# Performance work log

Measured on AMD Instinct MI355X. Metric: run time of the kernel, lower is better.

Reference implementation:

```python
import jax, jax.numpy as jnp
import numpy as np

N, E = 50000, 500000          # nodes per type, edges per message type
F_IN, H, L = 128, 128, 8      # input feat, hidden_size, num_labels
EPS, SLOPE = 1e-5, 0.01       # BatchNorm eps, LeakyReLU slope


def setup_inputs() -> dict:
    key = jax.random.key(0)
    ks = jax.random.split(key, 16)
    s = 0.05
    d = {}
    d["x_n0"] = jax.random.normal(ks[0], (N, F_IN), jnp.float32)
    d["x_n1"] = jax.random.normal(ks[1], (N, F_IN), jnp.float32)
    # stacked per-message-type SAGE params (3 message types), two layers
    d["Wn1"] = jax.random.normal(ks[2], (3, F_IN, H), jnp.float32) * s
    d["Ws1"] = jax.random.normal(ks[3], (3, F_IN, H), jnp.float32) * s
    d["Wu1"] = jax.random.normal(ks[4], (3, 2 * H, H), jnp.float32) * s
    d["Wn2"] = jax.random.normal(ks[5], (3, H, H), jnp.float32) * s
    d["Ws2"] = jax.random.normal(ks[6], (3, H, H), jnp.float32) * s
    d["Wu2"] = jax.random.normal(ks[7], (3, 2 * H, H), jnp.float32) * s
    for nm in ("bn1", "bs1", "bu1", "bn2", "bs2", "bu2"):
        d[nm] = jnp.zeros((3, H), jnp.float32)
    # per-node-type BatchNorm affine params (2 node types), two layers
    d["gamma1"] = jnp.ones((2, H), jnp.float32)
    d["beta1"] = jnp.zeros((2, H), jnp.float32)
    d["gamma2"] = jnp.ones((2, H), jnp.float32)
    d["beta2"] = jnp.zeros((2, H), jnp.float32)
    # per-node-type post-MP linear
    d["Wp"] = jax.random.normal(ks[8], (2, H, L), jnp.float32) * s
    d["bp"] = jnp.zeros((2, L), jnp.float32)
    # edge_index per message type: [2, E] with row0=src, row1=dst
    d["ei0"] = jax.random.randint(ks[9], (2, E), 0, N, jnp.int32)   # n0 -> n1
    d["ei1"] = jax.random.randint(ks[10], (2, E), 0, N, jnp.int32)  # n1 -> n0
    d["ei2"] = jax.random.randint(ks[11], (2, E), 0, N, jnp.int32)  # n0 -> n0
    return d


def _segment_mean(x, idx, n):
    s = jax.ops.segment_sum(x, idx, num_segments=n)
    c = jax.ops.segment_sum(jnp.ones((idx.shape[0], 1), x.dtype), idx, num_segments=n)
    return s / jnp.maximum(c, 1.0)


def _sage(x_src, x_dst, ei, Wn, bn, Ws, bs, Wu, bu):
    # gather source feats per edge, scatter-mean to dst, then linear branches
    agg = _segment_mean(x_src[ei[0]], ei[1], x_dst.shape[0])  # [N_dst, F]
    h = jnp.concatenate([agg @ Wn + bn, x_dst @ Ws + bs], axis=-1)
    return h @ Wu + bu


def _bn(x, g, b):
    m = x.mean(0)
    v = ((x - m) ** 2).mean(0)  # biased variance, as torch BN training mode
    return (x - m) * jax.lax.rsqrt(v + EPS) * g + b


def _lrelu(x):
    return jnp.where(x >= 0, x, SLOPE * x)


def _layer(x0, x1, ei0, ei1, ei2, Wn, bn, Ws, bs, Wu, bu, gamma, beta):
    m0 = _sage(x0, x1, ei0, Wn[0], bn[0], Ws[0], bs[0], Wu[0], bu[0])  # dst n1
    m1 = _sage(x1, x0, ei1, Wn[1], bn[1], Ws[1], bs[1], Wu[1], bu[1])  # dst n0
    m2 = _sage(x0, x0, ei2, Wn[2], bn[2], Ws[2], bs[2], Wu[2], bu[2])  # dst n0
    h0 = 0.5 * (m1 + m2)   # mean over the 2 message types targeting n0
    h1 = m0                # single message type for n1
    h0 = _lrelu(_bn(h0, gamma[0], beta[0]))
    h1 = _lrelu(_bn(h1, gamma[1], beta[1]))
    return h0, h1


def reference(x_n0, x_n1, Wn1, bn1, Ws1, bs1, Wu1, bu1,
              Wn2, bn2, Ws2, bs2, Wu2, bu2,
              gamma1, beta1, gamma2, beta2, Wp, bp, ei0, ei1, ei2):
    h0, h1 = _layer(x_n0, x_n1, ei0, ei1, ei2, Wn1, bn1, Ws1, bs1, Wu1, bu1, gamma1, beta1)
    h0, h1 = _layer(h0, h1, ei0, ei1, ei2, Wn2, bn2, Ws2, bs2, Wu2, bu2, gamma2, beta2)
    out0 = h0 @ Wp[0] + bp[0]
    out1 = h1 @ Wp[1] + bp[1]
    return jnp.stack([out0, out1])  # [2, N, L]
```

## Files before the change

### kernel.cpp

```cpp
#include <hip/hip_runtime.h>

#define LBL 8
#define NBMAX 128
#define BSH 9
#define BCAP 8192

typedef __attribute__((ext_vector_type(8))) short short8;
typedef __attribute__((ext_vector_type(4))) float f32x4;

__device__ __forceinline__ uint f2bf(float x) {
    uint u = __float_as_uint(x);
    return (u + 0x7fffu + ((u >> 16) & 1u)) >> 16;
}
__device__ __forceinline__ float bflo(uint v) { return __uint_as_float(v << 16); }
__device__ __forceinline__ float bfhi(uint v) { return __uint_as_float(v & 0xffff0000u); }

__device__ __forceinline__ void gload16(const ushort* g, ushort* l) {
    __builtin_amdgcn_global_load_lds((const __attribute__((address_space(1))) uint*)g,
                                     (__attribute__((address_space(3))) uint*)l, 16, 0, 0);
}

__global__ void f2b2(const float4* __restrict__ x0, const float4* __restrict__ x1,
                     uint2* __restrict__ o0, uint2* __restrict__ o1, int n4) {
    int y = blockIdx.y;
    const float4* in = y ? x1 : x0;
    uint2* out = y ? o1 : o0;
    int i = blockIdx.x * blockDim.x + threadIdx.x;
    int stride = gridDim.x * blockDim.x;
    for (; i < n4; i += stride) {
        float4 v = in[i];
        uint2 o;
        o.x = f2bf(v.x) | (f2bf(v.y) << 16);
        o.y = f2bf(v.z) | (f2bf(v.w) << 16);
        out[i] = o;
    }
}


__global__ void bhist3(const int* __restrict__ e0, const int* __restrict__ e1,
                       const int* __restrict__ e2, int E, int NB, int* __restrict__ bcnt) {
    int m = blockIdx.y;
    const int* dst = (m == 0 ? e0 : (m == 1 ? e1 : e2)) + E;
    __shared__ int h[NBMAX];
    int tid = threadIdx.x;
    if (tid < NB) h[tid] = 0;
    __syncthreads();
    int i = blockIdx.x * blockDim.x + tid, st = gridDim.x * blockDim.x;
    for (; i < E; i += st) atomicAdd(&h[dst[i] >> BSH], 1);
    __syncthreads();
    if (tid < NB && h[tid]) atomicAdd(&bcnt[m * NB + tid], h[tid]);
}

__global__ void bscan(const int* __restrict__ bcnt, int* __restrict__ bso,
                      int* __restrict__ gcur, int NB) {
    int m = threadIdx.x;
    if (m >= 3) return;
    int acc = 0;
    for (int b = 0; b < NB; ++b) {
        bso[m * (NB + 1) + b] = acc;
        gcur[m * NB + b] = acc;
        acc += bcnt[m * NB + b];
    }
    bso[m * (NB + 1) + NB] = acc;
}

#define BIN_CH 16
__global__ __launch_bounds__(256) void bin3(const int* __restrict__ e0, const int* __restrict__ e1,
                                            const int* __restrict__ e2, int E, int NB,
                                            int* __restrict__ gcur, uint* __restrict__ pairs) {
    int m = blockIdx.y;
    const int* eb = (m == 0 ? e0 : (m == 1 ? e1 : e2));
    const int* src = eb;
    const int* dst = eb + E;
    uint* pp = pairs + (size_t)m * E;
    int* gc = gcur + m * NB;
    __shared__ int h[NBMAX], base[NBMAX], pos[NBMAX];
    int tid = threadIdx.x;
    if (tid < NB) { h[tid] = 0; pos[tid] = 0; }
    __syncthreads();
    int i0 = blockIdx.x * (256 * BIN_CH);
    uint pk[BIN_CH];
    int bk[BIN_CH];
    #pragma unroll
    for (int u = 0; u < BIN_CH; ++u) {
        int i = i0 + u * 256 + tid;
        bk[u] = -1;
        if (i < E) {
            int s = src[i], d = dst[i];
            bk[u] = d >> BSH;
            pk[u] = (uint)s | ((uint)(d & ((1 << BSH) - 1)) << 16);
            atomicAdd(&h[bk[u]], 1);
        }
    }
    __syncthreads();
    if (tid < NB && h[tid]) base[tid] = atomicAdd(&gc[tid], h[tid]);
    __syncthreads();
    #pragma unroll
    for (int u = 0; u < BIN_CH; ++u) {
        if (bk[u] >= 0) {
            int p = base[bk[u]] + atomicAdd(&pos[bk[u]], 1);
            pp[p] = pk[u];
        }
    }
}

__global__ __launch_bounds__(256) void csr3(const uint* __restrict__ pairs, const int* __restrict__ bso,
                                            int E, int N, int NB,
                                            int* __restrict__ offs, ushort* __restrict__ srcs) {
    int m = blockIdx.y, b = blockIdx.x;
    const uint* pp = pairs + (size_t)m * E;
    int gstart = bso[m * (NB + 1) + b];
    int gend = bso[m * (NB + 1) + b + 1];
    int cnt = gend - gstart;
    if (cnt > BCAP) cnt = BCAP;
    int d0 = b << BSH;
    int dcnt = N - d0;
    if (dcnt > (1 << BSH)) dcnt = 1 << BSH;

    __shared__ int hist[1 << BSH], po[1 << BSH], off0[1 << BSH];
    __shared__ int lsort[BCAP];
    __shared__ int wsum[4];
    int tid = threadIdx.x;
    hist[tid] = 0;
    hist[tid + 256] = 0;
    __syncthreads();
    for (int i = tid; i < cnt; i += 256) atomicAdd(&hist[pp[gstart + i] >> 16], 1);
    __syncthreads();
    int a = hist[2 * tid], b2 = hist[2 * tid + 1];
    int s = a + b2;
    int lane = tid & 63, w = tid >> 6;
    #pragma unroll
    for (int o = 1; o < 64; o <<= 1) {
        int v = __shfl_up(s, o, 64);
        if (lane >= o) s += v;
    }
    if (lane == 63) wsum[w] = s;
    __syncthreads();
    int wp = 0;
    #pragma unroll
    for (int q = 0; q < 4; ++q)
        if (q < w) wp += wsum[q];
    int excl = wp + s - a - b2;
    off0[2 * tid] = excl; off0[2 * tid + 1] = excl + a;
    po[2 * tid] = excl;   po[2 * tid + 1] = excl + a;
    __syncthreads();
    for (int j = tid; j < dcnt; j += 256) offs[(size_t)m * (N + 1) + d0 + j] = gstart + off0[j];
    if (b == NB - 1 && tid == 0) offs[(size_t)m * (N + 1) + N] = bso[m * (NB + 1) + NB];
    for (int i = tid; i < cnt; i += 256) {
        uint e = pp[gstart + i];
        int p = atomicAdd(&po[e >> 16], 1);
        if (p < BCAP) lsort[p] = (int)(e & 0xffffu);
    }
    __syncthreads();
    for (int i = tid; i < cnt; i += 256) srcs[(size_t)m * E + gstart + i] = (ushort)lsort[i];
}

__global__ void agg3(const ushort* __restrict__ s0, const ushort* __restrict__ s1,
                     const ushort* __restrict__ s2,
                     uint* __restrict__ o0, uint* __restrict__ o1, uint* __restrict__ o2,
                     const int* __restrict__ offs, const ushort* __restrict__ srcs,
                     int n, int E) {
    int m = blockIdx.y;
    const uint4* x = (const uint4*)(m == 0 ? s0 : (m == 1 ? s1 : s2));
    uint4* o = (uint4*)(m == 0 ? o0 : (m == 1 ? o1 : o2));
    const int* off = offs + (size_t)m * (n + 1);
    const ushort* sl = srcs + (size_t)m * E;

    int tid = threadIdx.x;
    int l16 = tid & 15;
    int row = blockIdx.x * 16 + (tid >> 4);
    if (row >= n) return;
    int s = off[row], e = off[row + 1];
    float a0 = 0, a1 = 0, a2 = 0, a3 = 0, a4 = 0, a5 = 0, a6 = 0, a7 = 0;
    int i = s;
    for (; i + 3 < e; i += 4) {
        int j0 = sl[i], j1 = sl[i + 1], j2 = sl[i + 2], j3 = sl[i + 3];
        uint4 v0 = x[(size_t)j0 * 16 + l16];
        uint4 v1 = x[(size_t)j1 * 16 + l16];
        uint4 v2 = x[(size_t)j2 * 16 + l16];
        uint4 v3 = x[(size_t)j3 * 16 + l16];
        a0 += (bflo(v0.x) + bflo(v1.x)) + (bflo(v2.x) + bflo(v3.x));
        a1 += (bfhi(v0.x) + bfhi(v1.x)) + (bfhi(v2.x) + bfhi(v3.x));
        a2 += (bflo(v0.y) + bflo(v1.y)) + (bflo(v2.y) + bflo(v3.y));
        a3 += (bfhi(v0.y) + bfhi(v1.y)) + (bfhi(v2.y) + bfhi(v3.y));
        a4 += (bflo(v0.z) + bflo(v1.z)) + (bflo(v2.z) + bflo(v3.z));
        a5 += (bfhi(v0.z) + bfhi(v1.z)) + (bfhi(v2.z) + bfhi(v3.z));
        a6 += (bflo(v0.w) + bflo(v1.w)) + (bflo(v2.w) + bflo(v3.w));
        a7 += (bfhi(v0.w) + bfhi(v1.w)) + (bfhi(v2.w) + bfhi(v3.w));
    }
    for (; i < e; ++i) {
        uint4 v = x[(size_t)sl[i] * 16 + l16];
        a0 += bflo(v.x); a1 += bfhi(v.x);
        a2 += bflo(v.y); a3 += bfhi(v.y);
        a4 += bflo(v.z); a5 += bfhi(v.z);
        a6 += bflo(v.w); a7 += bfhi(v.w);
    }
    int d = e - s;
    float inv = 1.f / (float)(d > 0 ? d : 1);
    uint4 r;
    r.x = f2bf(a0 * inv) | (f2bf(a1 * inv) << 16);
    r.y = f2bf(a2 * inv) | (f2bf(a3 * inv) << 16);
    r.z = f2bf(a4 * inv) | (f2bf(a5 * inv) << 16);
    r.w = f2bf(a6 * inv) | (f2bf(a7 * inv) << 16);
    o[(size_t)row * 16 + l16] = r;
}

__global__ void fuseW(const float* __restrict__ Wn1, const float* __restrict__ Ws1,
                      const float* __restrict__ Wu1,
                      const float* __restrict__ Wn2, const float* __restrict__ Ws2,
                      const float* __restrict__ Wu2, ushort* __restrict__ FT) {
    int j5 = blockIdx.y;
    int l = j5 / 5, t = j5 - l * 5;
    const float* Wn = l ? Wn2 : Wn1;
    const float* Ws = l ? Ws2 : Ws1;
    const float* Wu = l ? Wu2 : Wu1;
    const float *A0, *B0, *A1 = nullptr, *B1 = nullptr;
    float al;
    switch (t) {
        case 0: A0 = Wn;          B0 = Wu;          al = 1.0f; break;
        case 1: A0 = Wn + 16384;  B0 = Wu + 32768;  al = 0.5f; break;
        case 2: A0 = Wn + 32768;  B0 = Wu + 65536;  al = 0.5f; break;
        case 3: A0 = Ws;          B0 = Wu + 16384;  al = 1.0f; break;
        default:
            A0 = Ws + 16384; B0 = Wu + 49152;
            A1 = Ws + 32768; B1 = Wu + 81920;
            al = 0.5f; break;
    }
    int i = blockIdx.x, j = threadIdx.x;
    float s0 = 0, s1 = 0, s2 = 0, s3 = 0;
    #pragma unroll 4
    for (int k = 0; k < 128; k += 4) {
        s0 += A0[i * 128 + k]     * B0[k * 128 + j];
        s1 += A0[i * 128 + k + 1] * B0[(k + 1) * 128 + j];
        s2 += A0[i * 128 + k + 2] * B0[(k + 2) * 128 + j];
        s3 += A0[i * 128 + k + 3] * B0[(k + 3) * 128 + j];
    }
    if (A1) {
        #pragma unroll 4
        for (int k = 0; k < 128; k += 4) {
            s0 += A1[i * 128 + k]     * B1[k * 128 + j];
            s1 += A1[i * 128 + k + 1] * B1[(k + 1) * 128 + j];
            s2 += A1[i * 128 + k + 2] * B1[(k + 2) * 128 + j];
            s3 += A1[i * 128 + k + 3] * B1[(k + 3) * 128 + j];
        }
    }
    float r = al * ((s0 + s1) + (s2 + s3));
    FT[(size_t)j5 * 16384 + j * 128 + i] = (ushort)f2bf(r);
}

__global__ void fuseB(const float* __restrict__ bn1, const float* __restrict__ bs1,
                      const float* __restrict__ bu1, const float* __restrict__ Wu1,
                      const float* __restrict__ bn2, const float* __restrict__ bs2,
                      const float* __restrict__ bu2, const float* __restrict__ Wu2,
                      float* __restrict__ FC) {
    int jb = blockIdx.x;
    int l = jb >> 1, which = jb & 1;
    const float* bn = l ? bn2 : bn1;
    const float* bs = l ? bs2 : bs1;
    const float* bu = l ? bu2 : bu1;
    const float* Wu = l ? Wu2 : Wu1;
    int j = threadIdx.x;
    float s = 0.f;
    if (which == 0) {
        s = bu[j];
        for (int k = 0; k < 128; ++k)
            s += bn[k] * Wu[k * 128 + j] + bs[k] * Wu[(128 + k) * 128 + j];
    } else {
        #pragma unroll
        for (int tt = 1; tt <= 2; ++tt) {
            const float* Wt = Wu + tt * 32768;
            float p = bu[tt * 128 + j];
            for (int k = 0; k < 128; ++k)
                p += bn[tt * 128 + k] * Wt[k * 128 + j] + bs[tt * 128 + k] * Wt[(128 + k) * 128 + j];
            s += 0.5f * p;
        }
    }
    FC[jb * 128 + j] = s;
}

__global__ __launch_bounds__(256) void gemm2_mfma(
    const ushort* __restrict__ Aq0, const ushort* __restrict__ Wq0,
    const ushort* __restrict__ Aq1, const ushort* __restrict__ Wq1,
    const ushort* __restrict__ Ap0, const ushort* __restrict__ Wp0,
    const ushort* __restrict__ Ap1, const ushort* __restrict__ Wp1,
    const ushort* __restrict__ Ap2, const ushort* __restrict__ Wp2,
    const float* __restrict__ biasq, const float* __restrict__ biasp,
    ushort* __restrict__ Cq, ushort* __restrict__ Cp, int M,
    float* __restrict__ STW) {
    __shared__ ushort As[2][64 * 128];
    int y = blockIdx.y;
    const float* bias = y ? biasp : biasq;
    ushort* C = y ? Cp : Cq;
    float* colsum = STW + (size_t)(blockIdx.x & 31) * 512 + (y ? 0 : 256);
    float* colsq = colsum + 128;

    int tid = threadIdx.x;
    int wid = tid >> 6;
    int lane = tid & 63;
    int l15 = lane & 15, lg = lane >> 4;
    int row0 = blockIdx.x * 64;
    int nIn = y ? 3 : 2;

    const ushort* Ax[3];
    const ushort* Wx[3];
    Ax[0] = y ? Ap0 : Aq0;  Wx[0] = y ? Wp0 : Wq0;
    Ax[1] = y ? Ap1 : Aq1;  Wx[1] = y ? Wp1 : Wq1;
    Ax[2] = Ap2;            Wx[2] = Wp2;

    auto stage = [&](const ushort* A, ushort* buf) {
        #pragma unroll
        for (int p = 0; p < 4; ++p) {
            int row = wid * 16 + p * 4 + (lane >> 4);
            int gr = row0 + row;
            if (gr > M - 1) gr = M - 1;
            const ushort* src = A + (size_t)gr * 128 + (((lane & 15) ^ (row & 7)) * 8);
            gload16(src, buf + (wid * 4 + p) * 512);
        }
    };

    f32x4 acc[4][2];
    #pragma unroll
    for (int rb = 0; rb < 4; ++rb)
        #pragma unroll
        for (int cb = 0; cb < 2; ++cb) acc[rb][cb] = (f32x4){0.f, 0.f, 0.f, 0.f};

    stage(Ax[0], As[0]);
    __syncthreads();
    int cur = 0;

    #pragma unroll
    for (int inp = 0; inp < 3; ++inp) {
        if (inp == 2 && nIn == 2) break;
        const ushort* W = Wx[inp];
        short8 bw[4][2];
        #pragma unroll
        for (int k0 = 0; k0 < 4; ++k0)
            #pragma unroll
            for (int cb = 0; cb < 2; ++cb)
                bw[k0][cb] = *(const short8*)(W + (size_t)(wid * 32 + cb * 16 + l15) * 128 + k0 * 32 + lg * 8);
        if (inp + 1 < nIn) stage(Ax[inp + 1], As[cur ^ 1]);
        #pragma unroll
        for (int k0 = 0; k0 < 4; ++k0) {
            short8 a[4];
            #pragma unroll
            for (int rb = 0; rb < 4; ++rb)
                a[rb] = *(const short8*)&As[cur][(rb * 16 + l15) * 128 + (((k0 * 4 + lg) ^ (l15 & 7)) * 8)];
            #pragma unroll
            for (int rb = 0; rb < 4; ++rb)
                #pragma unroll
                for (int cb = 0; cb < 2; ++cb)
                    acc[rb][cb] = __builtin_amdgcn_mfma_f32_16x16x32_bf16(a[rb], bw[k0][cb], acc[rb][cb], 0, 0, 0);
        }
        __syncthreads();
        cur ^= 1;
    }

    float ps[2] = {0.f, 0.f}, pq[2] = {0.f, 0.f};
    int colbase = wid * 32;
    ushort* T = As[0];
    #pragma unroll
    for (int cb = 0; cb < 2; ++cb) {
        int col = colbase + cb * 16 + l15;
        float b = bias[col];
        #pragma unroll
        for (int rb = 0; rb < 4; ++rb) {
            int lrow = rb * 16 + lg * 4;
            #pragma unroll
            for (int i = 0; i < 4; ++i) {
                float v = acc[rb][cb][i] + b;
                T[(lrow + i) * 128 + col] = (ushort)f2bf(v);
                if (row0 + lrow + i < M) {
                    ps[cb] += v;
                    pq[cb] += v * v;
                }
            }
        }
    }
    #pragma unroll
    for (int cb = 0; cb < 2; ++cb) {
        ps[cb] += __shfl_xor(ps[cb], 16, 64);
        ps[cb] += __shfl_xor(ps[cb], 32, 64);
        pq[cb] += __shfl_xor(pq[cb], 16, 64);
        pq[cb] += __shfl_xor(pq[cb], 32, 64);
    }
    if (lane < 16) {
        atomicAdd(&colsum[colbase + lane], ps[0]);
        atomicAdd(&colsq[colbase + lane], pq[0]);
        atomicAdd(&colsum[colbase + 16 + lane], ps[1]);
        atomicAdd(&colsq[colbase + 16 + lane], pq[1]);
    }
    __syncthreads();
    {
        int row = tid >> 2;
        int c0 = (tid & 3) * 32;
        int gr = row0 + row;
        if (gr < M) {
            uint4* dst = (uint4*)(C + (size_t)gr * 128 + c0);
            const uint4* src4 = (const uint4*)&T[row * 128 + c0];
            dst[0] = src4[0];
            dst[1] = src4[1];
            dst[2] = src4[2];
            dst[3] = src4[3];
        }
    }
}

__global__ void bn_fin2(float* __restrict__ STW, float* __restrict__ ST,
                        const float* __restrict__ g0, const float* __restrict__ b0,
                        const float* __restrict__ g1, const float* __restrict__ b1, int N) {
    int tid = threadIdx.x;
    int which = tid >> 7, c = tid & 127;
    float s = 0.f, q = 0.f;
    #pragma unroll 8
    for (int cp = 0; cp < 32; ++cp) {
        s += STW[(size_t)cp * 512 + which * 256 + c];
        q += STW[(size_t)cp * 512 + which * 256 + 128 + c];
    }
    #pragma unroll 8
    for (int cp = 0; cp < 32; ++cp) {
        STW[(size_t)cp * 512 + which * 256 + c] = 0.f;
        STW[(size_t)cp * 512 + which * 256 + 128 + c] = 0.f;
    }
    const float* g = which ? g1 : g0;
    const float* b = which ? b1 : b0;
    float m = s / (float)N;
    float v = q / (float)N - m * m;
    float rs = rsqrtf(v + 1e-5f);
    float sc = g[c] * rs;
    ST[512 + which * 256 + c] = sc;
    ST[640 + which * 256 + c] = b[c] - m * sc;
}

__global__ void bn_apply2(const ushort* __restrict__ Cp, ushort* __restrict__ X0b,
                          const ushort* __restrict__ Cq, ushort* __restrict__ X1b,
                          const float* __restrict__ ST, int n4) {
    int y = blockIdx.y;
    const uint2* in = (const uint2*)(y ? Cq : Cp);
    uint2* out = (uint2*)(y ? X1b : X0b);
    const float* sc = ST + 512 + y * 256;
    const float* sh = sc + 128;
    int i = blockIdx.x * blockDim.x + threadIdx.x;
    int stride = gridDim.x * blockDim.x;
    for (; i < n4; i += stride) {
        uint2 v = in[i];
        int cb = (i * 4) & 127;
        float4 s4 = *(const float4*)&sc[cb];
        float4 h4 = *(const float4*)&sh[cb];
        float y0 = bflo(v.x) * s4.x + h4.x;
        float y1 = bfhi(v.x) * s4.y + h4.y;
        float y2 = bflo(v.y) * s4.z + h4.z;
        float y3 = bfhi(v.y) * s4.w + h4.w;
        y0 = (y0 >= 0.f) ? y0 : 0.01f * y0;
        y1 = (y1 >= 0.f) ? y1 : 0.01f * y1;
        y2 = (y2 >= 0.f) ? y2 : 0.01f * y2;
        y3 = (y3 >= 0.f) ? y3 : 0.01f * y3;
        uint2 o;
        o.x = f2bf(y0) | (f2bf(y1) << 16);
        o.y = f2bf(y2) | (f2bf(y3) << 16);
        out[i] = o;
    }
}

__global__ void projbn2(const ushort* __restrict__ Cp, const ushort* __restrict__ Cq,
                        const float* __restrict__ ST,
                        const float* __restrict__ Wp, const float* __restrict__ bp,
                        float* __restrict__ out, int N) {
    int y = blockIdx.y;
    const uint* h = (const uint*)(y ? Cq : Cp);
    const float* W = Wp + y * 1024;
    const float* b = bp + y * 8;
    float* op = out + (size_t)y * N * 8;
    __shared__ float Wsh[1024];
    __shared__ float scs[128], shs[128];
    __shared__ float bsh[8];
    int tid = threadIdx.x;
    for (int i = tid; i < 1024; i += 256) Wsh[i] = W[i];
    if (tid < 128) {
        scs[tid] = ST[512 + y * 256 + tid];
        shs[tid] = ST[640 + y * 256 + tid];
    }
    if (tid < 8) bsh[tid] = b[tid];
    __syncthreads();
    int idx = blockIdx.x * 256 + tid;
    if (idx >= N * LBL) return;
    int r = idx >> 3, c = idx & 7;
    const uint* hr = h + (size_t)r * 64;
    float s = bsh[c];
    #pragma unroll
    for (int k2 = 0; k2 < 64; ++k2) {
        uint v = hr[k2];
        float xa = bflo(v) * scs[2 * k2] + shs[2 * k2];
        float xb = bfhi(v) * scs[2 * k2 + 1] + shs[2 * k2 + 1];
        xa = (xa >= 0.f) ? xa : 0.01f * xa;
        xb = (xb >= 0.f) ? xb : 0.01f * xb;
        s += xa * Wsh[(2 * k2) * 8 + c] + xb * Wsh[(2 * k2 + 1) * 8 + c];
    }
    op[idx] = s;
}


extern "C" void kernel_launch(void* const* d_in, const int* in_sizes, int n_in,
                              void* d_out, int out_size, void* d_ws, size_t ws_size,
                              hipStream_t stream) {
    const float* x0 = (const float*)d_in[0];
    const float* x1 = (const float*)d_in[1];
    const float* Wn1 = (const float*)d_in[2];
    const float* Ws1 = (const float*)d_in[3];
    const float* Wu1 = (const float*)d_in[4];
    const float* Wn2 = (const float*)d_in[5];
    const float* Ws2 = (const float*)d_in[6];
    const float* Wu2 = (const float*)d_in[7];
    const float* bnn[2] = {(const float*)d_in[8], (const float*)d_in[11]};
    const float* bss[2] = {(const float*)d_in[9], (const float*)d_in[12]};
    const float* buu[2] = {(const float*)d_in[10], (const float*)d_in[13]};
    const float* gam[2] = {(const float*)d_in[14], (const float*)d_in[16]};
    const float* bet[2] = {(const float*)d_in[15], (const float*)d_in[17]};
    const float* Wp = (const float*)d_in[18];
    const float* bp = (const float*)d_in[19];
    const int* ei[3] = {(const int*)d_in[20], (const int*)d_in[21], (const int*)d_in[22]};

    const int N = in_sizes[0] / 128;
    const int E = in_sizes[20] / 2;
    const int NB = (N + (1 << BSH) - 1) >> BSH;
    float* out = (float*)d_out;

    char* wp_ = (char*)d_ws;
    auto carve = [&](size_t bytes) {
        char* r = wp_;
        wp_ += (bytes + 255) & ~(size_t)255;
        return r;
    };
    size_t nodeB = (size_t)N * 128 * sizeof(ushort);
    ushort* Cp = (ushort*)carve(nodeB);
    ushort* Cq = (ushort*)carve(nodeB);
    ushort* Pb = (ushort*)carve(nodeB);
    ushort* Rb = (ushort*)carve(nodeB);
    ushort* Sb = (ushort*)carve(nodeB);
    ushort* X0b = (ushort*)carve(nodeB);
    ushort* X1b = (ushort*)carve(nodeB);
    ushort* x0b = (ushort*)carve(nodeB);
    ushort* x1b = (ushort*)carve(nodeB);
    ushort* FT = (ushort*)carve(10 * 16384 * 2);
    float* FC = (float*)carve(4 * 128 * 4);
    float* ST = (float*)carve(1024 * 4);
    float* STW = (float*)carve(32 * 512 * 4);
    int* offs = (int*)carve((size_t)3 * (N + 1) * 4);
    ushort* srcs = (ushort*)carve((size_t)3 * E * 2);
    int* bcnt = (int*)carve((size_t)3 * NB * 4);
    int* bso = (int*)carve((size_t)3 * (NB + 1) * 4);
    int* gcur = (int*)carve((size_t)3 * NB * 4);
    uint* pairs = (uint*)Cp;

    const int ag = (N + 15) / 16;
    const int gg = (N + 63) / 64;
    const int pg = (N * LBL + 255) / 256;
    const int bg = (E + 256 * BIN_CH - 1) / (256 * BIN_CH);

    f2b2<<<dim3(1024, 2), 256, 0, stream>>>((const float4*)x0, (const float4*)x1,
                                            (uint2*)x0b, (uint2*)x1b, N * 32);

    hipMemsetAsync(bcnt, 0, (size_t)3 * NB * 4, stream);
    hipMemsetAsync(STW, 0, 32 * 512 * 4, stream);
    bhist3<<<dim3(512, 3), 256, 0, stream>>>(ei[0], ei[1], ei[2], E, NB, bcnt);
    bscan<<<1, 64, 0, stream>>>(bcnt, bso, gcur, NB);
    bin3<<<dim3(bg, 3), 256, 0, stream>>>(ei[0], ei[1], ei[2], E, NB, gcur, pairs);
    csr3<<<dim3(NB, 3), 256, 0, stream>>>(pairs, bso, E, N, NB, offs, srcs);

    fuseW<<<dim3(128, 10), 128, 0, stream>>>(Wn1, Ws1, Wu1, Wn2, Ws2, Wu2, FT);
    fuseB<<<4, 128, 0, stream>>>(bnn[0], bss[0], buu[0], Wu1, bnn[1], bss[1], buu[1], Wu2, FC);

    const ushort* srcS[2][3] = {{x0b, x1b, x0b}, {X0b, X1b, X0b}};
    const ushort* dstX[2][2] = {{x0b, x1b}, {X0b, X1b}};

    for (int l = 0; l < 2; ++l) {
        const ushort* FA0T = FT + (size_t)(l * 5 + 0) * 16384;
        const ushort* FA1T = FT + (size_t)(l * 5 + 1) * 16384;
        const ushort* FA2T = FT + (size_t)(l * 5 + 2) * 16384;
        const ushort* FB1T = FT + (size_t)(l * 5 + 3) * 16384;
        const ushort* FB0T = FT + (size_t)(l * 5 + 4) * 16384;
        const float* fcH1 = FC + (l * 2 + 0) * 128;
        const float* fcH0 = FC + (l * 2 + 1) * 128;

        agg3<<<dim3(ag, 3), 256, 0, stream>>>(srcS[l][0], srcS[l][1], srcS[l][2],
                                              (uint*)Pb, (uint*)Rb, (uint*)Sb,
                                              offs, srcs, N, E);

        gemm2_mfma<<<dim3(gg, 2), 256, 0, stream>>>(
            Pb, FA0T, dstX[l][1], FB1T,
            Rb, FA1T, Sb, FA2T, dstX[l][0], FB0T,
            fcH1, fcH0, Cq, Cp, N, STW);

        bn_fin2<<<1, 256, 0, stream>>>(STW, ST, gam[l], bet[l], gam[l] + 128, bet[l] + 128, N);
        if (l == 0)
            bn_apply2<<<dim3(1024, 2), 256, 0, stream>>>(Cp, X0b, Cq, X1b, ST, N * 32);
    }

    projbn2<<<dim3(pg, 2), 256, 0, stream>>>(Cp, Cq, ST, Wp, bp, out, N);
}
```

Baseline: 299.3 us.

## Merge prep kernels into one launch and fold BN finalize into consumers

Combines the float-to-bf16 conversion, destination histogram, weight fusion and bias fusion into a single block-partitioned prep kernel to cut launch count. Removes the separate single-block BN finalize kernel by having bn_apply2 and projbn2 each reduce the 32 partial stat slices themselves. Gives each layer its own stats buffer so nothing has to be zeroed between layers. The cost is redundant per-block stat reductions and halving bn_apply2's grid.

```diff
diff --git a/kernel.cpp b/kernel.cpp
--- a/kernel.cpp
+++ b/kernel.cpp
@@ -20,35 +20,109 @@
                                      (__attribute__((address_space(3))) uint*)l, 16, 0, 0);
 }
 
-__global__ void f2b2(const float4* __restrict__ x0, const float4* __restrict__ x1,
-                     uint2* __restrict__ o0, uint2* __restrict__ o1, int n4) {
-    int y = blockIdx.y;
-    const float4* in = y ? x1 : x0;
-    uint2* out = y ? o1 : o0;
-    int i = blockIdx.x * blockDim.x + threadIdx.x;
-    int stride = gridDim.x * blockDim.x;
-    for (; i < n4; i += stride) {
-        float4 v = in[i];
-        uint2 o;
-        o.x = f2bf(v.x) | (f2bf(v.y) << 16);
-        o.y = f2bf(v.z) | (f2bf(v.w) << 16);
-        out[i] = o;
-    }
-}
-
-
-__global__ void bhist3(const int* __restrict__ e0, const int* __restrict__ e1,
-                       const int* __restrict__ e2, int E, int NB, int* __restrict__ bcnt) {
-    int m = blockIdx.y;
-    const int* dst = (m == 0 ? e0 : (m == 1 ? e1 : e2)) + E;
+__global__ __launch_bounds__(256) void prep(
+    const float4* __restrict__ x0, const float4* __restrict__ x1,
+    uint2* __restrict__ o0, uint2* __restrict__ o1, int n4,
+    const int* __restrict__ e0, const int* __restrict__ e1, const int* __restrict__ e2,
+    int E, int NB, int* __restrict__ bcnt,
+    const float* __restrict__ Wn1, const float* __restrict__ Ws1, const float* __restrict__ Wu1,
+    const float* __restrict__ Wn2, const float* __restrict__ Ws2, const float* __restrict__ Wu2,
+    ushort* __restrict__ FT,
+    const float* __restrict__ bn1, const float* __restrict__ bs1, const float* __restrict__ bu1,
+    const float* __restrict__ bn2, const float* __restrict__ bs2, const float* __restrict__ bu2,
+    float* __restrict__ FC) {
     __shared__ int h[NBMAX];
+    int b = blockIdx.x;
     int tid = threadIdx.x;
-    if (tid < NB) h[tid] = 0;
-    __syncthreads();
-    int i = blockIdx.x * blockDim.x + tid, st = gridDim.x * blockDim.x;
-    for (; i < E; i += st) atomicAdd(&h[dst[i] >> BSH], 1);
-    __syncthreads();
-    if (tid < NB && h[tid]) atomicAdd(&bcnt[m * NB + tid], h[tid]);
+
+    if (b < 1024) {
+        int y = b >> 9;
+        const float4* in = y ? x1 : x0;
+        uint2* out = y ? o1 : o0;
+        int i = (b & 511) * 256 + tid;
+        int stride = 512 * 256;
+        for (; i < n4; i += stride) {
+            float4 v = in[i];
+            uint2 o;
+            o.x = f2bf(v.x) | (f2bf(v.y) << 16);
+            o.y = f2bf(v.z) | (f2bf(v.w) << 16);
+            out[i] = o;
+        }
+    } else if (b < 2560) {
+        int bb = b - 1024;
+        int m = bb / 512, sub = bb - m * 512;
+        const int* dst = (m == 0 ? e0 : (m == 1 ? e1 : e2)) + E;
+        if (tid < NB) h[tid] = 0;
+        __syncthreads();
+        int i = sub * 256 + tid, st = 512 * 256;
+        for (; i < E; i += st) atomicAdd(&h[dst[i] >> BSH], 1);
+        __syncthreads();
+        if (tid < NB && h[tid]) atomicAdd(&bcnt[m * NB + tid], h[tid]);
+    } else if (b < 3200) {
+        int bb = b - 2560;
+        int j5 = bb >> 6, rem = bb & 63;
+        int l = j5 / 5, t = j5 - l * 5;
+        const float* Wn = l ? Wn2 : Wn1;
+        const float* Ws = l ? Ws2 : Ws1;
+        const float* Wu = l ? Wu2 : Wu1;
+        const float *A0, *B0, *A1 = nullptr, *B1 = nullptr;
+        float al;
+        switch (t) {
+            case 0: A0 = Wn;          B0 = Wu;          al = 1.0f; break;
+            case 1: A0 = Wn + 16384;  B0 = Wu + 32768;  al = 0.5f; break;
+            case 2: A0 = Wn + 32768;  B0 = Wu + 65536;  al = 0.5f; break;
+            case 3: A0 = Ws;          B0 = Wu + 16384;  al = 1.0f; break;
+            default:
+                A0 = Ws + 16384; B0 = Wu + 49152;
+                A1 = Ws + 32768; B1 = Wu + 81920;
+                al = 0.5f; break;
+        }
+        int i = rem * 2 + (tid >> 7);
+        int j = tid & 127;
+        float s0 = 0, s1 = 0, s2 = 0, s3 = 0;
+        #pragma unroll 4
+        for (int k = 0; k < 128; k += 4) {
+            s0 += A0[i * 128 + k]     * B0[k * 128 + j];
+            s1 += A0[i * 128 + k + 1] * B0[(k + 1) * 128 + j];
+            s2 += A0[i * 128 + k + 2] * B0[(k + 2) * 128 + j];
+            s3 += A0[i * 128 + k + 3] * B0[(k + 3) * 128 + j];
+        }
+        if (A1) {
+            #pragma unroll 4
+            for (int k = 0; k < 128; k += 4) {
+                s0 += A1[i * 128 + k]     * B1[k * 128 + j];
+                s1 += A1[i * 128 + k + 1] * B1[(k + 1) * 128 + j];
+                s2 += A1[i * 128 + k + 2] * B1[(k + 2) * 128 + j];
+                s3 += A1[i * 128 + k + 3] * B1[(k + 3) * 128 + j];
+            }
+        }
+        float r = al * ((s0 + s1) + (s2 + s3));
+        FT[(size_t)j5 * 16384 + j * 128 + i] = (ushort)f2bf(r);
+    } else {
+        int jb = (b - 3200) * 2 + (tid >> 7);
+        int l = jb >> 1, which = jb & 1;
+        const float* bn = l ? bn2 : bn1;
+        const float* bs = l ? bs2 : bs1;
+        const float* bu = l ? bu2 : bu1;
+        const float* Wu = l ? Wu2 : Wu1;
+        int j = tid & 127;
+        float s = 0.f;
+        if (which == 0) {
+            s = bu[j];
+            for (int k = 0; k < 128; ++k)
+                s += bn[k] * Wu[k * 128 + j] + bs[k] * Wu[(128 + k) * 128 + j];
+        } else {
+            #pragma unroll
+            for (int tt = 1; tt <= 2; ++tt) {
+                const float* Wt = Wu + tt * 32768;
+                float p = bu[tt * 128 + j];
+                for (int k = 0; k < 128; ++k)
+                    p += bn[tt * 128 + k] * Wt[k * 128 + j] + bs[tt * 128 + k] * Wt[(128 + k) * 128 + j];
+                s += 0.5f * p;
+            }
+        }
+        FC[jb * 128 + j] = s;
+    }
 }
 
 __global__ void bscan(const int* __restrict__ bcnt, int* __restrict__ bso,
@@ -205,79 +279,6 @@
     o[(size_t)row * 16 + l16] = r;
 }
 
-__global__ void fuseW(const float* __restrict__ Wn1, const float* __restrict__ Ws1,
-                      const float* __restrict__ Wu1,
-                      const float* __restrict__ Wn2, const float* __restrict__ Ws2,
-                      const float* __restrict__ Wu2, ushort* __restrict__ FT) {
-    int j5 = blockIdx.y;
-    int l = j5 / 5, t = j5 - l * 5;
-    const float* Wn = l ? Wn2 : Wn1;
-    const float* Ws = l ? Ws2 : Ws1;
-    const float* Wu = l ? Wu2 : Wu1;
-    const float *A0, *B0, *A1 = nullptr, *B1 = nullptr;
-    float al;
-    switch (t) {
-        case 0: A0 = Wn;          B0 = Wu;          al = 1.0f; break;
-        case 1: A0 = Wn + 16384;  B0 = Wu + 32768;  al = 0.5f; break;
-        case 2: A0 = Wn + 32768;  B0 = Wu + 65536;  al = 0.5f; break;
-        case 3: A0 = Ws;          B0 = Wu + 16384;  al = 1.0f; break;
-        default:
-            A0 = Ws + 16384; B0 = Wu + 49152;
-            A1 = Ws + 32768; B1 = Wu + 81920;
-            al = 0.5f; break;
-    }
-    int i = blockIdx.x, j = threadIdx.x;
-    float s0 = 0, s1 = 0, s2 = 0, s3 = 0;
-    #pragma unroll 4
-    for (int k = 0; k < 128; k += 4) {
-        s0 += A0[i * 128 + k]     * B0[k * 128 + j];
-        s1 += A0[i * 128 + k + 1] * B0[(k + 1) * 128 + j];
-        s2 += A0[i * 128 + k + 2] * B0[(k + 2) * 128 + j];
-        s3 += A0[i * 128 + k + 3] * B0[(k + 3) * 128 + j];
-    }
-    if (A1) {
-        #pragma unroll 4
-        for (int k = 0; k < 128; k += 4) {
-            s0 += A1[i * 128 + k]     * B1[k * 128 + j];
-            s1 += A1[i * 128 + k + 1] * B1[(k + 1) * 128 + j];
-            s2 += A1[i * 128 + k + 2] * B1[(k + 2) * 128 + j];
-            s3 += A1[i * 128 + k + 3] * B1[(k + 3) * 128 + j];
-        }
-    }
-    float r = al * ((s0 + s1) + (s2 + s3));
-    FT[(size_t)j5 * 16384 + j * 128 + i] = (ushort)f2bf(r);
-}
-
-__global__ void fuseB(const float* __restrict__ bn1, const float* __restrict__ bs1,
-                      const float* __restrict__ bu1, const float* __restrict__ Wu1,
-                      const float* __restrict__ bn2, const float* __restrict__ bs2,
-                      const float* __restrict__ bu2, const float* __restrict__ Wu2,
-                      float* __restrict__ FC) {
-    int jb = blockIdx.x;
-    int l = jb >> 1, which = jb & 1;
-    const float* bn = l ? bn2 : bn1;
-    const float* bs = l ? bs2 : bs1;
-    const float* bu = l ? bu2 : bu1;
-    const float* Wu = l ? Wu2 : Wu1;
-    int j = threadIdx.x;
-    float s = 0.f;
-    if (which == 0) {
-        s = bu[j];
-        for (int k = 0; k < 128; ++k)
-            s += bn[k] * Wu[k * 128 + j] + bs[k] * Wu[(128 + k) * 128 + j];
-    } else {
-        #pragma unroll
-        for (int tt = 1; tt <= 2; ++tt) {
-            const float* Wt = Wu + tt * 32768;
-            float p = bu[tt * 128 + j];
-            for (int k = 0; k < 128; ++k)
-                p += bn[tt * 128 + k] * Wt[k * 128 + j] + bs[tt * 128 + k] * Wt[(128 + k) * 128 + j];
-            s += 0.5f * p;
-        }
-    }
-    FC[jb * 128 + j] = s;
-}
-
 __global__ __launch_bounds__(256) void gemm2_mfma(
     const ushort* __restrict__ Aq0, const ushort* __restrict__ Wq0,
     const ushort* __restrict__ Aq1, const ushort* __restrict__ Wq1,
@@ -405,47 +406,39 @@
     }
 }
 
-__global__ void bn_fin2(float* __restrict__ STW, float* __restrict__ ST,
-                        const float* __restrict__ g0, const float* __restrict__ b0,
-                        const float* __restrict__ g1, const float* __restrict__ b1, int N) {
-    int tid = threadIdx.x;
-    int which = tid >> 7, c = tid & 127;
-    float s = 0.f, q = 0.f;
-    #pragma unroll 8
-    for (int cp = 0; cp < 32; ++cp) {
-        s += STW[(size_t)cp * 512 + which * 256 + c];
-        q += STW[(size_t)cp * 512 + which * 256 + 128 + c];
-    }
-    #pragma unroll 8
-    for (int cp = 0; cp < 32; ++cp) {
-        STW[(size_t)cp * 512 + which * 256 + c] = 0.f;
-        STW[(size_t)cp * 512 + which * 256 + 128 + c] = 0.f;
-    }
-    const float* g = which ? g1 : g0;
-    const float* b = which ? b1 : b0;
-    float m = s / (float)N;
-    float v = q / (float)N - m * m;
-    float rs = rsqrtf(v + 1e-5f);
-    float sc = g[c] * rs;
-    ST[512 + which * 256 + c] = sc;
-    ST[640 + which * 256 + c] = b[c] - m * sc;
-}
-
 __global__ void bn_apply2(const ushort* __restrict__ Cp, ushort* __restrict__ X0b,
                           const ushort* __restrict__ Cq, ushort* __restrict__ X1b,
-                          const float* __restrict__ ST, int n4) {
+                          const float* __restrict__ STWl,
+                          const float* __restrict__ gam, const float* __restrict__ bet,
+                          int N, int n4) {
     int y = blockIdx.y;
     const uint2* in = (const uint2*)(y ? Cq : Cp);
     uint2* out = (uint2*)(y ? X1b : X0b);
-    const float* sc = ST + 512 + y * 256;
-    const float* sh = sc + 128;
-    int i = blockIdx.x * blockDim.x + threadIdx.x;
+    __shared__ float scs[128], shs[128];
+    int tid = threadIdx.x;
+    if (tid < 128) {
+        const float* base = STWl + (y ? 256 : 0);
+        float s = 0.f, q = 0.f;
+        #pragma unroll 8
+        for (int cp = 0; cp < 32; ++cp) {
+            s += base[cp * 512 + tid];
+            q += base[cp * 512 + 128 + tid];
+        }
+        float m = s / (float)N;
+        float v = q / (float)N - m * m;
+        float rs = rsqrtf(v + 1e-5f);
+        float sc = gam[y * 128 + tid] * rs;
+        scs[tid] = sc;
+        shs[tid] = bet[y * 128 + tid] - m * sc;
+    }
+    __syncthreads();
+    int i = blockIdx.x * blockDim.x + tid;
     int stride = gridDim.x * blockDim.x;
     for (; i < n4; i += stride) {
         uint2 v = in[i];
         int cb = (i * 4) & 127;
-        float4 s4 = *(const float4*)&sc[cb];
-        float4 h4 = *(const float4*)&sh[cb];
+        float4 s4 = *(const float4*)&scs[cb];
+        float4 h4 = *(const float4*)&shs[cb];
         float y0 = bflo(v.x) * s4.x + h4.x;
         float y1 = bfhi(v.x) * s4.y + h4.y;
         float y2 = bflo(v.y) * s4.z + h4.z;
@@ -462,9 +455,10 @@
 }
 
 __global__ void projbn2(const ushort* __restrict__ Cp, const ushort* __restrict__ Cq,
-                        const float* __restrict__ ST,
+                        const float* __restrict__ STWl,
+                        const float* __restrict__ gam, const float* __restrict__ bet,
                         const float* __restrict__ Wp, const float* __restrict__ bp,
-                        float* __restrict__ out, int N) {
+                        float* __restrict__ out, int NN, int N) {
     int y = blockIdx.y;
     const uint* h = (const uint*)(y ? Cq : Cp);
     const float* W = Wp + y * 1024;
@@ -476,8 +470,19 @@
     int tid = threadIdx.x;
     for (int i = tid; i < 1024; i += 256) Wsh[i] = W[i];
     if (tid < 128) {
-        scs[tid] = ST[512 + y * 256 + tid];
-        shs[tid] = ST[640 + y * 256 + tid];
+        const float* base = STWl + (y ? 256 : 0);
+        float s = 0.f, q = 0.f;
+        #pragma unroll 8
+        for (int cp = 0; cp < 32; ++cp) {
+            s += base[cp * 512 + tid];
+            q += base[cp * 512 + 128 + tid];
+        }
+        float m = s / (float)NN;
+        float v = q / (float)NN - m * m;
+        float rs = rsqrtf(v + 1e-5f);
+        float sc = gam[y * 128 + tid] * rs;
+        scs[tid] = sc;
+        shs[tid] = bet[y * 128 + tid] - m * sc;
     }
     if (tid < 8) bsh[tid] = b[tid];
     __syncthreads();
@@ -542,8 +547,7 @@
     ushort* x1b = (ushort*)carve(nodeB);
     ushort* FT = (ushort*)carve(10 * 16384 * 2);
     float* FC = (float*)carve(4 * 128 * 4);
-    float* ST = (float*)carve(1024 * 4);
-    float* STW = (float*)carve(32 * 512 * 4);
+    float* STW = (float*)carve(2 * 32 * 512 * 4);
     int* offs = (int*)carve((size_t)3 * (N + 1) * 4);
     ushort* srcs = (ushort*)carve((size_t)3 * E * 2);
     int* bcnt = (int*)carve((size_t)3 * NB * 4);
@@ -556,18 +560,18 @@
     const int pg = (N * LBL + 255) / 256;
     const int bg = (E + 256 * BIN_CH - 1) / (256 * BIN_CH);
 
-    f2b2<<<dim3(1024, 2), 256, 0, stream>>>((const float4*)x0, (const float4*)x1,
-                                            (uint2*)x0b, (uint2*)x1b, N * 32);
-
     hipMemsetAsync(bcnt, 0, (size_t)3 * NB * 4, stream);
-    hipMemsetAsync(STW, 0, 32 * 512 * 4, stream);
-    bhist3<<<dim3(512, 3), 256, 0, stream>>>(ei[0], ei[1], ei[2], E, NB, bcnt);
+    hipMemsetAsync(STW, 0, (size_t)2 * 32 * 512 * 4, stream);
+
+    prep<<<3202, 256, 0, stream>>>(
+        (const float4*)x0, (const float4*)x1, (uint2*)x0b, (uint2*)x1b, N * 32,
+        ei[0], ei[1], ei[2], E, NB, bcnt,
+        Wn1, Ws1, Wu1, Wn2, Ws2, Wu2, FT,
+        bnn[0], bss[0], buu[0], bnn[1], bss[1], buu[1], FC);
+
     bscan<<<1, 64, 0, stream>>>(bcnt, bso, gcur, NB);
     bin3<<<dim3(bg, 3), 256, 0, stream>>>(ei[0], ei[1], ei[2], E, NB, gcur, pairs);
     csr3<<<dim3(NB, 3), 256, 0, stream>>>(pairs, bso, E, N, NB, offs, srcs);
-
-    fuseW<<<dim3(128, 10), 128, 0, stream>>>(Wn1, Ws1, Wu1, Wn2, Ws2, Wu2, FT);
-    fuseB<<<4, 128, 0, stream>>>(bnn[0], bss[0], buu[0], Wu1, bnn[1], bss[1], buu[1], Wu2, FC);
 
     const ushort* srcS[2][3] = {{x0b, x1b, x0b}, {X0b, X1b, X0b}};
     const ushort* dstX[2][2] = {{x0b, x1b}, {X0b, X1b}};
@@ -580,6 +584,7 @@
         const ushort* FB0T = FT + (size_t)(l * 5 + 4) * 16384;
         const float* fcH1 = FC + (l * 2 + 0) * 128;
         const float* fcH0 = FC + (l * 2 + 1) * 128;
+        float* STWl = STW + (size_t)l * 32 * 512;
 
         agg3<<<dim3(ag, 3), 256, 0, stream>>>(srcS[l][0], srcS[l][1], srcS[l][2],
                                               (uint*)Pb, (uint*)Rb, (uint*)Sb,
@@ -588,12 +593,13 @@
         gemm2_mfma<<<dim3(gg, 2), 256, 0, stream>>>(
             Pb, FA0T, dstX[l][1], FB1T,
             Rb, FA1T, Sb, FA2T, dstX[l][0], FB0T,
-            fcH1, fcH0, Cq, Cp, N, STW);
-
-        bn_fin2<<<1, 256, 0, stream>>>(STW, ST, gam[l], bet[l], gam[l] + 128, bet[l] + 128, N);
+            fcH1, fcH0, Cq, Cp, N, STWl);
+
         if (l == 0)
-            bn_apply2<<<dim3(1024, 2), 256, 0, stream>>>(Cp, X0b, Cq, X1b, ST, N * 32);
-    }
-
-    projbn2<<<dim3(pg, 2), 256, 0, stream>>>(Cp, Cq, ST, Wp, bp, out, N);
-}
+            bn_apply2<<<dim3(512, 2), 256, 0, stream>>>(Cp, X0b, Cq, X1b, STWl,
+                                                        gam[0], bet[0], N, N * 32);
+    }
+
+    projbn2<<<dim3(pg, 2), 256, 0, stream>>>(Cp, Cq, STW + 32 * 512,
+                                             gam[1], bet[1], Wp, bp, out, N, N);
+}
```

Measured after the change: 285.7 us. -4.5%, faster.
